# Kernel tuning notes

Measured on AMD Instinct MI355X. Metric: run time of the kernel, lower is better.

The kernel has to match this reference:

```python
import jax, jax.numpy as jnp
import numpy as np

DIM = 128
NUM_HEADS = 4
WS = 7          # window_size
SHIFT = 3       # shift_size
H = W = 56
B = 64
SCALE = DIM ** (-0.5)  # note: module scales by dim**-0.5, not head_dim**-0.5
NEG_INF = -1e9


def _make_attn_mask():
    # Static Swin shifted-window mask, built with numpy at trace time.
    img = np.zeros((H, W), dtype=np.float32)
    slices = (slice(0, -WS), slice(-WS, -SHIFT), slice(-SHIFT, None))
    cnt = 0
    for hs in slices:
        for ws_ in slices:
            img[hs, ws_] = cnt
            cnt += 1
    # window partition: [nW, WS*WS]
    m = img.reshape(H // WS, WS, W // WS, WS).transpose(0, 2, 1, 3).reshape(-1, WS * WS)
    am = m[:, None, :] - m[:, :, None]          # [nW, N, N]
    am = np.where(am != 0, NEG_INF, 0.0).astype(np.float32)
    return jnp.asarray(am)


def _window_partition(x):
    # x: [B, H, W, C] -> [B*nW, WS*WS, C]
    Bx, Hx, Wx, C = x.shape
    x = x.reshape(Bx, Hx // WS, WS, Wx // WS, WS, C)
    x = x.transpose(0, 1, 3, 2, 4, 5)
    return x.reshape(-1, WS * WS, C)


def _window_reverse(w):
    # w: [B*nW, WS*WS, C] -> [B, H, W, C]
    C = w.shape[-1]
    x = w.reshape(B, H // WS, W // WS, WS, WS, C)
    x = x.transpose(0, 1, 3, 2, 4, 5)
    return x.reshape(B, H, W, C)


def setup_inputs() -> dict:
    key = jax.random.key(0)
    k1, k2, k3 = jax.random.split(key, 3)
    x = jax.random.normal(k1, (B, H, W, DIM), dtype=jnp.float32)
    qkv_w = jax.random.normal(k2, (DIM, 3 * DIM), dtype=jnp.float32) * 0.02
    qkv_b = jnp.zeros((3 * DIM,), dtype=jnp.float32)
    proj_w = jax.random.normal(k3, (DIM, DIM), dtype=jnp.float32) * 0.02
    proj_b = jnp.zeros((DIM,), dtype=jnp.float32)
    return {"x": x, "qkv_w": qkv_w, "qkv_b": qkv_b, "proj_w": proj_w, "proj_b": proj_b}


def reference(x, qkv_w, qkv_b, proj_w, proj_b):
    attn_mask = _make_attn_mask()                       # [nW, N, N]
    N = WS * WS
    hd = DIM // NUM_HEADS

    shifted = jnp.roll(x, shift=(-SHIFT, -SHIFT), axis=(1, 2))
    xw = _window_partition(shifted)                     # [B*nW, N, C]

    qkv = xw @ qkv_w + qkv_b                            # [B*nW, N, 3C]
    qkv = qkv.reshape(-1, N, 3, NUM_HEADS, hd)
    q, k, v = qkv[:, :, 0], qkv[:, :, 1], qkv[:, :, 2]  # [B*nW, N, h, hd]

    attn = jnp.einsum('wnhd,wmhd->whnm', q, k) * SCALE  # [B*nW, h, N, N]
    nW = attn_mask.shape[0]
    attn = attn.reshape(B, nW, NUM_HEADS, N, N) + attn_mask[None, :, None, :, :]
    attn = jax.nn.softmax(attn.reshape(-1, NUM_HEADS, N, N), axis=-1)

    out = jnp.einsum('whnm,wmhd->wnhd', attn, v).reshape(-1, N, DIM)
    out = out @ proj_w + proj_b                         # [B*nW, N, C]

    shifted_out = _window_reverse(out)                  # [B, H, W, C]
    return jnp.roll(shifted_out, shift=(SHIFT, SHIFT), axis=(1, 2))
```

## Files before the change

kernel.cpp:

```cpp
#include <hip/hip_runtime.h>
#include <hip/hip_bf16.h>


#define NTOK 49
#define QS (0.08838834764831844f * 1.4426950408889634f)

typedef __bf16 bf16x8 __attribute__((ext_vector_type(8)));
typedef __bf16 bf16x2 __attribute__((ext_vector_type(2)));
typedef float  f32x4  __attribute__((ext_vector_type(4)));
typedef unsigned int u32x4 __attribute__((ext_vector_type(4)));

__device__ __forceinline__ f32x4 mfma_bf16(bf16x8 a, bf16x8 b, f32x4 c) {
  return __builtin_amdgcn_mfma_f32_16x16x32_bf16(a, b, c, 0, 0, 0);
}

__device__ __forceinline__ unsigned int pack2(float lo, float hi) {
  bf16x2 t; t[0] = (__bf16)lo; t[1] = (__bf16)hi;
  return __builtin_bit_cast(unsigned int, t);
}

__device__ __forceinline__ bf16x8 cvt8(f32x4 a, f32x4 b) {
  bf16x8 r;
#pragma unroll
  for (int j = 0; j < 4; ++j) { r[j] = (__bf16)a[j]; r[4 + j] = (__bf16)b[j]; }
  return r;
}

__device__ __forceinline__ bf16x8 push_frag(unsigned int t0w0, unsigned int t0w1,
                                            unsigned int t1w0, unsigned int t1w1,
                                            int addrA, int addrB, int g0, int g1) {
  unsigned int a0 = g0 ? t1w0 : t0w0;
  unsigned int a1 = g0 ? t1w1 : t0w1;
  unsigned int b0 = g0 ? t0w0 : t1w0;
  unsigned int b1 = g0 ? t0w1 : t1w1;
  unsigned int rA0 = (unsigned int)__builtin_amdgcn_ds_permute(addrA, (int)a0);
  unsigned int rA1 = (unsigned int)__builtin_amdgcn_ds_permute(addrA, (int)a1);
  unsigned int rB0 = (unsigned int)__builtin_amdgcn_ds_permute(addrB, (int)b0);
  unsigned int rB1 = (unsigned int)__builtin_amdgcn_ds_permute(addrB, (int)b1);
  u32x4 u;
  u[0] = g1 ? rB0 : rA0;
  u[1] = g1 ? rB1 : rA1;
  u[2] = g1 ? rA0 : rB0;
  u[3] = g1 ? rA1 : rB1;
  return __builtin_bit_cast(bf16x8, u);
}

__device__ __forceinline__ int regid(int t, int wh, int ww) {
  int i = t / 7;
  int j = t - i * 7;
  int rh = (wh == 7) ? ((i < 4) ? 1 : 2) : 0;
  int rw = (ww == 7) ? ((j < 4) ? 1 : 2) : 0;
  return rh * 3 + rw;
}

__global__ void repack_w(const float* __restrict__ w, ushort* __restrict__ packed,
                         int ncol, int scale_below, float scale) {
  int ctg  = blockIdx.x;
  int kt   = threadIdx.x >> 6;
  int lane = threadIdx.x & 63;
  int col  = ctg * 16 + (lane & 15);
  int k0   = kt * 32 + (lane >> 4) * 8;
  float s  = (ctg < scale_below) ? scale : 1.0f;
  ushort* dst = packed + (size_t)((ctg * 4 + kt) * 64 + lane) * 8;
#pragma unroll
  for (int j = 0; j < 8; ++j) {
    __bf16 h = (__bf16)(w[(size_t)(k0 + j) * ncol + col] * s);
    dst[j] = __builtin_bit_cast(ushort, h);
  }
}

__global__ __launch_bounds__(256, 3)
void swin_fused(const float* __restrict__ x,
                const float* __restrict__ qkv_b,
                const float* __restrict__ proj_b,
                const ushort* __restrict__ pqkv,
                const ushort* __restrict__ pproj,
                float* __restrict__ out)
{
  __shared__ alignas(16) ushort ao[64 * 136];

  const int wid = blockIdx.x;
  const int b   = wid >> 6;
  const int wh  = (wid >> 3) & 7;
  const int ww  = wid & 7;
  const int tid  = threadIdx.x;
  const int wave = tid >> 6;
  const int lane = tid & 63;
  const int c    = lane & 15;
  const int g    = lane >> 4;
  const int g0   = g & 1;
  const int g1   = g >> 1;
  const int addrA = (((2 * g0 + g1) << 4) | c) << 2;
  const int addrB = (((2 * (1 - g0) + g1) << 4) | c) << 2;
  const f32x4 zf = {0.f, 0.f, 0.f, 0.f};

  bf16x8 xf[4][4];
#pragma unroll
  for (int nt = 0; nt < 4; ++nt) {
    int token = nt * 16 + c;
    bool valid = token < NTOK;
    int tc = valid ? token : 0;
    int i = tc / 7;
    int j = tc - i * 7;
    int gh = wh * 7 + i + 3; if (gh >= 56) gh -= 56;
    int gw = ww * 7 + j + 3; if (gw >= 56) gw -= 56;
    const float* src = x + (((size_t)((b * 56 + gh) * 56 + gw)) << 7) + g * 8;
#pragma unroll
    for (int kt = 0; kt < 4; ++kt) {
      f32x4 lo = *reinterpret_cast<const f32x4*>(src + kt * 32);
      f32x4 hi = *reinterpret_cast<const f32x4*>(src + kt * 32 + 4);
      bf16x8 v = cvt8(lo, hi);
      xf[nt][kt] = valid ? v : bf16x8{};
    }
  }

  unsigned int pkk[2][4][2], pkq[2][4][2], pkv[4][2][2];

#pragma unroll
  for (int o = 0; o < 2; ++o) {
    f32x4 qc[2][4];
#pragma unroll
    for (int mt = 0; mt < 2; ++mt)
#pragma unroll
      for (int nt = 0; nt < 4; ++nt) qc[mt][nt] = zf;
#pragma unroll
    for (int kt = 0; kt < 4; ++kt) {
      bf16x8 w0 = *reinterpret_cast<const bf16x8*>(
          pqkv + (size_t)((((o ? 0 : 8) + wave * 2 + 0) * 4 + kt) * 64 + lane) * 8);
      bf16x8 w1 = *reinterpret_cast<const bf16x8*>(
          pqkv + (size_t)((((o ? 0 : 8) + wave * 2 + 1) * 4 + kt) * 64 + lane) * 8);
#pragma unroll
      for (int nt = 0; nt < 4; ++nt) {
        qc[0][nt] = mfma_bf16(w0, xf[nt][kt], qc[0][nt]);
        qc[1][nt] = mfma_bf16(w1, xf[nt][kt], qc[1][nt]);
      }
    }
    float bscale = o ? QS : 1.0f;
    int bbase = (o ? 0 : 128) + wave * 32;
#pragma unroll
    for (int mt = 0; mt < 2; ++mt)
#pragma unroll
      for (int r = 0; r < 4; ++r) {
        float bv = qkv_b[bbase + mt * 16 + g * 4 + r] * bscale;
#pragma unroll
        for (int nt = 0; nt < 4; ++nt) qc[mt][nt][r] += bv;
      }
#pragma unroll
    for (int mt = 0; mt < 2; ++mt)
#pragma unroll
      for (int nt = 0; nt < 4; ++nt) {
        unsigned int* dst = o ? pkq[mt][nt] : pkk[mt][nt];
        dst[0] = pack2(qc[mt][nt][0], qc[mt][nt][1]);
        dst[1] = pack2(qc[mt][nt][2], qc[mt][nt][3]);
      }
  }

  {
    f32x4 vc[4][2];
#pragma unroll
    for (int mt = 0; mt < 4; ++mt) { vc[mt][0] = zf; vc[mt][1] = zf; }
#pragma unroll
    for (int kt = 0; kt < 4; ++kt) {
      bf16x8 w0 = *reinterpret_cast<const bf16x8*>(
          pqkv + (size_t)(((16 + wave * 2 + 0) * 4 + kt) * 64 + lane) * 8);
      bf16x8 w1 = *reinterpret_cast<const bf16x8*>(
          pqkv + (size_t)(((16 + wave * 2 + 1) * 4 + kt) * 64 + lane) * 8);
#pragma unroll
      for (int mt = 0; mt < 4; ++mt) {
        vc[mt][0] = mfma_bf16(xf[mt][kt], w0, vc[mt][0]);
        vc[mt][1] = mfma_bf16(xf[mt][kt], w1, vc[mt][1]);
      }
    }
    float bv0 = qkv_b[256 + wave * 32 + c];
    float bv1 = qkv_b[256 + wave * 32 + 16 + c];
#pragma unroll
    for (int mt = 0; mt < 4; ++mt)
#pragma unroll
      for (int r = 0; r < 4; ++r) { vc[mt][0][r] += bv0; vc[mt][1][r] += bv1; }
#pragma unroll
    for (int mt = 0; mt < 4; ++mt)
#pragma unroll
      for (int nv = 0; nv < 2; ++nv) {
        pkv[mt][nv][0] = pack2(vc[mt][nv][0], vc[mt][nv][1]);
        pkv[mt][nv][1] = pack2(vc[mt][nv][2], vc[mt][nv][3]);
      }
  }

  bf16x8 ka[4], qa[4];
#pragma unroll
  for (int t4 = 0; t4 < 4; ++t4) {
    ka[t4] = push_frag(pkk[0][t4][0], pkk[0][t4][1], pkk[1][t4][0], pkk[1][t4][1],
                       addrA, addrB, g0, g1);
    qa[t4] = push_frag(pkq[0][t4][0], pkq[0][t4][1], pkq[1][t4][0], pkq[1][t4][1],
                       addrA, addrB, g0, g1);
  }
  f32x4 st[4][4];
#pragma unroll
  for (int m = 0; m < 4; ++m)
#pragma unroll
    for (int n = 0; n < 4; ++n)
      st[m][n] = mfma_bf16(ka[m], qa[n], zf);

  int ridq[4];
#pragma unroll
  for (int n = 0; n < 4; ++n) ridq[n] = regid(n * 16 + c, wh, ww);
  int ridk[4][4];
#pragma unroll
  for (int m = 0; m < 4; ++m)
#pragma unroll
    for (int r = 0; r < 4; ++r) {
      int kt_ = m * 16 + g * 4 + r;
      ridk[m][r] = (kt_ < NTOK) ? regid(kt_, wh, ww) : -1;
    }

  unsigned int pkp[4][4][2];
#pragma unroll
  for (int n = 0; n < 4; ++n) {
    float ev[4][4];
    float mx = -1e30f;
#pragma unroll
    for (int m = 0; m < 4; ++m)
#pragma unroll
      for (int r = 0; r < 4; ++r) {
        float v = (ridk[m][r] == ridq[n]) ? st[m][n][r] : -1e30f;
        ev[m][r] = v;
        mx = fmaxf(mx, v);
      }
    mx = fmaxf(mx, __shfl_xor(mx, 16));
    mx = fmaxf(mx, __shfl_xor(mx, 32));
    float sm = 0.f;
#pragma unroll
    for (int m = 0; m < 4; ++m)
#pragma unroll
      for (int r = 0; r < 4; ++r) {
        float e = exp2f(ev[m][r] - mx);
        ev[m][r] = e;
        sm += e;
      }
    sm += __shfl_xor(sm, 16);
    sm += __shfl_xor(sm, 32);
    float rinv = __fdividef(1.f, sm);
#pragma unroll
    for (int m = 0; m < 4; ++m) {
      pkp[m][n][0] = pack2(ev[m][0] * rinv, ev[m][1] * rinv);
      pkp[m][n][1] = pack2(ev[m][2] * rinv, ev[m][3] * rinv);
    }
  }

  f32x4 po[4][2];
#pragma unroll
  for (int m = 0; m < 4; ++m) { po[m][0] = zf; po[m][1] = zf; }
#pragma unroll
  for (int kt = 0; kt < 2; ++kt) {
    bf16x8 vf0 = push_frag(pkv[2 * kt][0][0], pkv[2 * kt][0][1],
                           pkv[2 * kt + 1][0][0], pkv[2 * kt + 1][0][1],
                           addrA, addrB, g0, g1);
    bf16x8 vf1 = push_frag(pkv[2 * kt][1][0], pkv[2 * kt][1][1],
                           pkv[2 * kt + 1][1][0], pkv[2 * kt + 1][1][1],
                           addrA, addrB, g0, g1);
#pragma unroll
    for (int m = 0; m < 4; ++m) {
      bf16x8 pa = push_frag(pkp[2 * kt][m][0], pkp[2 * kt][m][1],
                            pkp[2 * kt + 1][m][0], pkp[2 * kt + 1][m][1],
                            addrA, addrB, g0, g1);
      po[m][0] = mfma_bf16(pa, vf0, po[m][0]);
      po[m][1] = mfma_bf16(pa, vf1, po[m][1]);
    }
  }

#pragma unroll
  for (int m = 0; m < 4; ++m)
#pragma unroll
    for (int nv = 0; nv < 2; ++nv)
#pragma unroll
      for (int r = 0; r < 4; ++r) {
        __bf16 h = (__bf16)po[m][nv][r];
        ao[(m * 16 + g * 4 + r) * 136 + wave * 32 + nv * 16 + c] =
            __builtin_bit_cast(ushort, h);
      }
  __syncthreads();

  f32x4 acc2[4][2];
#pragma unroll
  for (int m = 0; m < 4; ++m) { acc2[m][0] = zf; acc2[m][1] = zf; }
#pragma unroll
  for (int kt = 0; kt < 4; ++kt) {
    bf16x8 b20 = *reinterpret_cast<const bf16x8*>(
        pproj + (size_t)(((wave * 2 + 0) * 4 + kt) * 64 + lane) * 8);
    bf16x8 b21 = *reinterpret_cast<const bf16x8*>(
        pproj + (size_t)(((wave * 2 + 1) * 4 + kt) * 64 + lane) * 8);
#pragma unroll
    for (int m = 0; m < 4; ++m) {
      bf16x8 af = *reinterpret_cast<const bf16x8*>(&ao[(m * 16 + c) * 136 + kt * 32 + g * 8]);
      acc2[m][0] = mfma_bf16(af, b20, acc2[m][0]);
      acc2[m][1] = mfma_bf16(af, b21, acc2[m][1]);
    }
  }
  float pb0 = proj_b[wave * 32 + c];
  float pb1 = proj_b[wave * 32 + 16 + c];

#pragma unroll
  for (int m = 0; m < 4; ++m)
#pragma unroll
    for (int r = 0; r < 4; ++r) {
      int token = m * 16 + g * 4 + r;
      if (token < NTOK) {
        int i = token / 7;
        int j = token - i * 7;
        int oh = wh * 7 + i + 3; if (oh >= 56) oh -= 56;
        int ow = ww * 7 + j + 3; if (ow >= 56) ow -= 56;
        float* dst = out + (((size_t)((b * 56 + oh) * 56 + ow)) << 7) + wave * 32;
        dst[c]      = acc2[m][0][r] + pb0;
        dst[16 + c] = acc2[m][1][r] + pb1;
      }
    }
}

extern "C" void kernel_launch(void* const* d_in, const int* in_sizes, int n_in,
                              void* d_out, int out_size, void* d_ws, size_t ws_size,
                              hipStream_t stream) {
  const float* x      = (const float*)d_in[0];
  const float* qkv_w  = (const float*)d_in[1];
  const float* qkv_b  = (const float*)d_in[2];
  const float* proj_w = (const float*)d_in[3];
  const float* proj_b = (const float*)d_in[4];
  float* out = (float*)d_out;

  ushort* pqkv  = (ushort*)d_ws;
  ushort* pproj = pqkv + 49152;

  repack_w<<<24, 256, 0, stream>>>(qkv_w, pqkv, 384, 8, QS);
  repack_w<<<8, 256, 0, stream>>>(proj_w, pproj, 128, 0, 1.0f);
  swin_fused<<<4096, 256, 0, stream>>>(x, qkv_b, proj_b, pqkv, pproj, out);
}
```

Measured before the change: 259.1 us.

## Eliminate ds_permute fragment shuffles via permuted-K MFMA layouts and mask-via-MFMA

Replaces the cross-lane ds_permute repacking of K, Q, V and P fragments by packing accumulator outputs directly into MFMA operand registers. This works because the K dimension of the dot product may be permuted consistently across both operands. The per-element region mask compare is replaced by an extra MFMA over one-hot bf16 mask fragments, which adds a large negative bias to cross-region scores. Softmax normalisation is deferred to after the PV product, and the AV MFMA is transposed so each lane writes contiguous uint2 values to LDS. The risks are bf16 precision in the mask encoding and extra MFMA work for the mask.

```diff
diff --git a/kernel.cpp b/kernel.cpp
--- a/kernel.cpp
+++ b/kernel.cpp
@@ -24,25 +24,6 @@
 #pragma unroll
   for (int j = 0; j < 4; ++j) { r[j] = (__bf16)a[j]; r[4 + j] = (__bf16)b[j]; }
   return r;
-}
-
-__device__ __forceinline__ bf16x8 push_frag(unsigned int t0w0, unsigned int t0w1,
-                                            unsigned int t1w0, unsigned int t1w1,
-                                            int addrA, int addrB, int g0, int g1) {
-  unsigned int a0 = g0 ? t1w0 : t0w0;
-  unsigned int a1 = g0 ? t1w1 : t0w1;
-  unsigned int b0 = g0 ? t0w0 : t1w0;
-  unsigned int b1 = g0 ? t0w1 : t1w1;
-  unsigned int rA0 = (unsigned int)__builtin_amdgcn_ds_permute(addrA, (int)a0);
-  unsigned int rA1 = (unsigned int)__builtin_amdgcn_ds_permute(addrA, (int)a1);
-  unsigned int rB0 = (unsigned int)__builtin_amdgcn_ds_permute(addrB, (int)b0);
-  unsigned int rB1 = (unsigned int)__builtin_amdgcn_ds_permute(addrB, (int)b1);
-  u32x4 u;
-  u[0] = g1 ? rB0 : rA0;
-  u[1] = g1 ? rB1 : rA1;
-  u[2] = g1 ? rA0 : rB0;
-  u[3] = g1 ? rA1 : rB1;
-  return __builtin_bit_cast(bf16x8, u);
 }
 
 __device__ __forceinline__ int regid(int t, int wh, int ww) {
@@ -88,10 +69,6 @@
   const int lane = tid & 63;
   const int c    = lane & 15;
   const int g    = lane >> 4;
-  const int g0   = g & 1;
-  const int g1   = g >> 1;
-  const int addrA = (((2 * g0 + g1) << 4) | c) << 2;
-  const int addrB = (((2 * (1 - g0) + g1) << 4) | c) << 2;
   const f32x4 zf = {0.f, 0.f, 0.f, 0.f};
 
   bf16x8 xf[4][4];
@@ -114,7 +91,7 @@
     }
   }
 
-  unsigned int pkk[2][4][2], pkq[2][4][2], pkv[4][2][2];
+  bf16x8 kf[4], qf[4], vf[2][2];
 
 #pragma unroll
   for (int o = 0; o < 2; ++o) {
@@ -146,13 +123,15 @@
         for (int nt = 0; nt < 4; ++nt) qc[mt][nt][r] += bv;
       }
 #pragma unroll
-    for (int mt = 0; mt < 2; ++mt)
-#pragma unroll
-      for (int nt = 0; nt < 4; ++nt) {
-        unsigned int* dst = o ? pkq[mt][nt] : pkk[mt][nt];
-        dst[0] = pack2(qc[mt][nt][0], qc[mt][nt][1]);
-        dst[1] = pack2(qc[mt][nt][2], qc[mt][nt][3]);
-      }
+    for (int t = 0; t < 4; ++t) {
+      u32x4 u;
+      u[0] = pack2(qc[0][t][0], qc[0][t][1]);
+      u[1] = pack2(qc[0][t][2], qc[0][t][3]);
+      u[2] = pack2(qc[1][t][0], qc[1][t][1]);
+      u[3] = pack2(qc[1][t][2], qc[1][t][3]);
+      if (o) qf[t] = __builtin_bit_cast(bf16x8, u);
+      else   kf[t] = __builtin_bit_cast(bf16x8, u);
+    }
   }
 
   {
@@ -178,106 +157,84 @@
 #pragma unroll
       for (int r = 0; r < 4; ++r) { vc[mt][0][r] += bv0; vc[mt][1][r] += bv1; }
 #pragma unroll
-    for (int mt = 0; mt < 4; ++mt)
+    for (int kt = 0; kt < 2; ++kt)
 #pragma unroll
       for (int nv = 0; nv < 2; ++nv) {
-        pkv[mt][nv][0] = pack2(vc[mt][nv][0], vc[mt][nv][1]);
-        pkv[mt][nv][1] = pack2(vc[mt][nv][2], vc[mt][nv][3]);
-      }
-  }
-
-  bf16x8 ka[4], qa[4];
-#pragma unroll
-  for (int t4 = 0; t4 < 4; ++t4) {
-    ka[t4] = push_frag(pkk[0][t4][0], pkk[0][t4][1], pkk[1][t4][0], pkk[1][t4][1],
-                       addrA, addrB, g0, g1);
-    qa[t4] = push_frag(pkq[0][t4][0], pkq[0][t4][1], pkq[1][t4][0], pkq[1][t4][1],
-                       addrA, addrB, g0, g1);
-  }
-  f32x4 st[4][4];
-#pragma unroll
-  for (int m = 0; m < 4; ++m)
-#pragma unroll
-    for (int n = 0; n < 4; ++n)
-      st[m][n] = mfma_bf16(ka[m], qa[n], zf);
-
-  int ridq[4];
-#pragma unroll
-  for (int n = 0; n < 4; ++n) ridq[n] = regid(n * 16 + c, wh, ww);
-  int ridk[4][4];
-#pragma unroll
-  for (int m = 0; m < 4; ++m)
-#pragma unroll
-    for (int r = 0; r < 4; ++r) {
-      int kt_ = m * 16 + g * 4 + r;
-      ridk[m][r] = (kt_ < NTOK) ? regid(kt_, wh, ww) : -1;
-    }
-
-  unsigned int pkp[4][4][2];
+        u32x4 u;
+        u[0] = pack2(vc[2 * kt][nv][0], vc[2 * kt][nv][1]);
+        u[1] = pack2(vc[2 * kt][nv][2], vc[2 * kt][nv][3]);
+        u[2] = pack2(vc[2 * kt + 1][nv][0], vc[2 * kt + 1][nv][1]);
+        u[3] = pack2(vc[2 * kt + 1][nv][2], vc[2 * kt + 1][nv][3]);
+        vf[kt][nv] = __builtin_bit_cast(bf16x8, u);
+      }
+  }
+
+  bf16x8 mk[4];
+#pragma unroll
+  for (int t = 0; t < 4; ++t) {
+    int tok = t * 16 + c;
+    int rk = (tok < NTOK) ? regid(tok, wh, ww) : 99;
+    int d = rk - g * 4;
+    unsigned long long mm =
+        ((unsigned)d < 4u) ? (0x4180ull << (d * 16)) : 0ull;
+    u32x4 u = {(unsigned int)mm, (unsigned int)(mm >> 32), 0u, 0u};
+    mk[t] = __builtin_bit_cast(bf16x8, u);
+  }
+
+  bf16x8 ppf[2][4];
+  float rinv[4];
 #pragma unroll
   for (int n = 0; n < 4; ++n) {
-    float ev[4][4];
+    f32x4 stn[4];
+#pragma unroll
+    for (int m = 0; m < 4; ++m) {
+      stn[m] = mfma_bf16(mk[m], mk[n], zf);
+      stn[m] = mfma_bf16(kf[m], qf[n], stn[m]);
+    }
     float mx = -1e30f;
 #pragma unroll
     for (int m = 0; m < 4; ++m)
 #pragma unroll
-      for (int r = 0; r < 4; ++r) {
-        float v = (ridk[m][r] == ridq[n]) ? st[m][n][r] : -1e30f;
-        ev[m][r] = v;
-        mx = fmaxf(mx, v);
-      }
+      for (int r = 0; r < 4; ++r) mx = fmaxf(mx, stn[m][r]);
     mx = fmaxf(mx, __shfl_xor(mx, 16));
     mx = fmaxf(mx, __shfl_xor(mx, 32));
+    float e[4][4];
     float sm = 0.f;
 #pragma unroll
     for (int m = 0; m < 4; ++m)
 #pragma unroll
       for (int r = 0; r < 4; ++r) {
-        float e = exp2f(ev[m][r] - mx);
-        ev[m][r] = e;
-        sm += e;
+        float ev = exp2f(stn[m][r] - mx);
+        e[m][r] = ev;
+        sm += ev;
       }
     sm += __shfl_xor(sm, 16);
     sm += __shfl_xor(sm, 32);
-    float rinv = __fdividef(1.f, sm);
-#pragma unroll
-    for (int m = 0; m < 4; ++m) {
-      pkp[m][n][0] = pack2(ev[m][0] * rinv, ev[m][1] * rinv);
-      pkp[m][n][1] = pack2(ev[m][2] * rinv, ev[m][3] * rinv);
-    }
-  }
-
-  f32x4 po[4][2];
-#pragma unroll
-  for (int m = 0; m < 4; ++m) { po[m][0] = zf; po[m][1] = zf; }
-#pragma unroll
-  for (int kt = 0; kt < 2; ++kt) {
-    bf16x8 vf0 = push_frag(pkv[2 * kt][0][0], pkv[2 * kt][0][1],
-                           pkv[2 * kt + 1][0][0], pkv[2 * kt + 1][0][1],
-                           addrA, addrB, g0, g1);
-    bf16x8 vf1 = push_frag(pkv[2 * kt][1][0], pkv[2 * kt][1][1],
-                           pkv[2 * kt + 1][1][0], pkv[2 * kt + 1][1][1],
-                           addrA, addrB, g0, g1);
-#pragma unroll
-    for (int m = 0; m < 4; ++m) {
-      bf16x8 pa = push_frag(pkp[2 * kt][m][0], pkp[2 * kt][m][1],
-                            pkp[2 * kt + 1][m][0], pkp[2 * kt + 1][m][1],
-                            addrA, addrB, g0, g1);
-      po[m][0] = mfma_bf16(pa, vf0, po[m][0]);
-      po[m][1] = mfma_bf16(pa, vf1, po[m][1]);
-    }
-  }
-
-#pragma unroll
-  for (int m = 0; m < 4; ++m)
-#pragma unroll
-    for (int nv = 0; nv < 2; ++nv)
-#pragma unroll
-      for (int r = 0; r < 4; ++r) {
-        __bf16 h = (__bf16)po[m][nv][r];
-        ao[(m * 16 + g * 4 + r) * 136 + wave * 32 + nv * 16 + c] =
-            __builtin_bit_cast(ushort, h);
-      }
+    rinv[n] = __fdividef(1.f, sm);
+#pragma unroll
+    for (int kt = 0; kt < 2; ++kt) {
+      u32x4 u;
+      u[0] = pack2(e[2 * kt][0], e[2 * kt][1]);
+      u[1] = pack2(e[2 * kt][2], e[2 * kt][3]);
+      u[2] = pack2(e[2 * kt + 1][0], e[2 * kt + 1][1]);
+      u[3] = pack2(e[2 * kt + 1][2], e[2 * kt + 1][3]);
+      ppf[kt][n] = __builtin_bit_cast(bf16x8, u);
+    }
+  }
+
+#pragma unroll
+  for (int nv = 0; nv < 2; ++nv)
+#pragma unroll
+    for (int n = 0; n < 4; ++n) {
+      f32x4 po = mfma_bf16(vf[0][nv], ppf[0][n], zf);
+      po = mfma_bf16(vf[1][nv], ppf[1][n], po);
+      float ri = rinv[n];
+      uint2 w;
+      w.x = pack2(po[0] * ri, po[1] * ri);
+      w.y = pack2(po[2] * ri, po[3] * ri);
+      *reinterpret_cast<uint2*>(
+          &ao[(n * 16 + c) * 136 + wave * 32 + nv * 16 + g * 4]) = w;
+    }
   __syncthreads();
 
   f32x4 acc2[4][2];
```

New measurement: 270.5 us. 1.04x slower.
